# Kernel optimization log

Hardware: AMD Instinct MI355X
Metric: run time of the kernel (lower is better)

Reference implementation:

```python
import jax, jax.numpy as jnp
import numpy as np

B = 32768
IN_DIM = 768
HIDDENS = [2048, 1024, 512]
EMBED_DIM = 128
NUM_EMB = 1024
DEPTH = 3


def setup_inputs() -> dict:
    key = jax.random.key(0)
    ks = jax.random.split(key, 20)
    d = {"x": jax.random.normal(ks[0], (B, IN_DIM), dtype=jnp.float32)}
    # Encoder: in -> h0 -> h1 -> h2 -> embed  (weights stored as [in, out])
    enc_dims = [IN_DIM] + HIDDENS + [EMBED_DIM]
    for i in range(4):
        fan_in = enc_dims[i]
        d[f"enc_W{i+1}"] = jax.random.normal(ks[1 + i], (enc_dims[i], enc_dims[i + 1]), dtype=jnp.float32) / np.sqrt(fan_in)
        d[f"enc_b{i+1}"] = jnp.zeros((enc_dims[i + 1],), dtype=jnp.float32)
    # Decoder: embed -> h0 -> h1 -> h2 -> in
    dec_dims = [EMBED_DIM] + HIDDENS + [IN_DIM]
    for i in range(4):
        fan_in = dec_dims[i]
        d[f"dec_W{i+1}"] = jax.random.normal(ks[5 + i], (dec_dims[i], dec_dims[i + 1]), dtype=jnp.float32) / np.sqrt(fan_in)
        d[f"dec_b{i+1}"] = jnp.zeros((dec_dims[i + 1],), dtype=jnp.float32)
    # Codebook (nn.Embedding weight, initialized ~ N(0,1) as in the module)
    d["codebook"] = jax.random.normal(ks[9], (NUM_EMB, EMBED_DIM), dtype=jnp.float32)
    return d


def _encoder(x, W1, b1, W2, b2, W3, b3, W4, b4):
    x = jax.nn.relu(x @ W1 + b1)
    x = jax.nn.relu(x @ W2 + b2)
    x = jax.nn.relu(x @ W3 + b3)
    return x @ W4 + b4


def _decoder(x, W1, b1, W2, b2, W3, b3, W4, b4):
    x = jax.nn.relu(x @ W1 + b1)
    x = jax.nn.relu(x @ W2 + b2)
    x = jax.nn.relu(x @ W3 + b3)
    return x @ W4 + b4


def reference(x,
              enc_W1, enc_b1, enc_W2, enc_b2, enc_W3, enc_b3, enc_W4, enc_b4,
              dec_W1, dec_b1, dec_W2, dec_b2, dec_W3, dec_b3, dec_W4, dec_b4,
              codebook):
    z = _encoder(x, enc_W1, enc_b1, enc_W2, enc_b2, enc_W3, enc_b3, enc_W4, enc_b4)
    z_det = jax.lax.stop_gradient(z)

    cb_sq = jnp.sum(codebook * codebook, axis=1)  # [K]
    residue = z_det
    z_hat = jnp.zeros_like(z_det)
    codes = []
    for _ in range(DEPTH):  # residual quantization loop
        # squared L2 distances [B, K]
        dist = (jnp.sum(residue * residue, axis=1, keepdims=True)
                + cb_sq
                - 2.0 * residue @ codebook.T)
        idx = jnp.argmin(dist, axis=1)          # [B]
        codes.append(idx)
        z_hat = z_hat + codebook[idx]           # gather codebook vectors
        residue = z_det - z_hat
    all_codes = jnp.stack(codes, axis=1)        # [B, DEPTH] int

    # straight-through estimator: forward uses z_hat, grad flows through z
    z_flow = z + jax.lax.stop_gradient(z_hat - z)
    x_recon = _decoder(z_flow, dec_W1, dec_b1, dec_W2, dec_b2, dec_W3, dec_b3, dec_W4, dec_b4)
    return (x_recon, all_codes)
```

## Files before the change

kernel.cpp:

```cpp
#include <hip/hip_runtime.h>

#define FLT_MAX_C 3.402823466e+38f

typedef __attribute__((ext_vector_type(8))) __bf16 bf16x8;
typedef __attribute__((ext_vector_type(4))) float f32x4;

static __device__ __forceinline__ ushort f2bf(float x) {
    union { float f; unsigned u; } v; v.f = x;
    unsigned r = (v.u + 0x7FFFu + ((v.u >> 16) & 1u)) >> 16;
    return (ushort)r;
}

template<bool RELU>
__device__ __forceinline__ void gemm_f32_dev(
    const float* __restrict__ A, const float* __restrict__ W,
    const float* __restrict__ bias, float* __restrict__ C, int K, int N)
{
    __shared__ float As[8][128];
    __shared__ float Bs[8][132];
    const int tid = threadIdx.x;
    const int bm = blockIdx.y << 7;
    const int bn = blockIdx.x << 7;

    const int la_row = tid >> 1;
    const int la_k   = (tid & 1) << 2;
    const int lb_row = tid >> 5;
    const int lb_col = (tid & 31) << 2;
    const int tm4 = (tid >> 4) << 2;
    const int tn4 = (tid & 15) << 2;

    float acc[8][8];
    #pragma unroll
    for (int i = 0; i < 8; ++i)
        #pragma unroll
        for (int j = 0; j < 8; ++j) acc[i][j] = 0.f;

    const float* aptr = A + (size_t)(bm + la_row) * K + la_k;
    const float* bptr = W + (size_t)lb_row * N + bn + lb_col;

    float4 av = *(const float4*)(aptr);
    float4 bv = *(const float4*)(bptr);

    for (int k0 = 0; k0 < K; k0 += 8) {
        __syncthreads();
        As[la_k + 0][la_row] = av.x;
        As[la_k + 1][la_row] = av.y;
        As[la_k + 2][la_row] = av.z;
        As[la_k + 3][la_row] = av.w;
        *(float4*)(&Bs[lb_row][lb_col]) = bv;
        __syncthreads();
        if (k0 + 8 < K) {
            av = *(const float4*)(aptr + k0 + 8);
            bv = *(const float4*)(bptr + (size_t)(k0 + 8) * N);
        }
        #pragma unroll
        for (int kk = 0; kk < 8; ++kk) {
            float a[8], b[8];
            *(float4*)(a)     = *(const float4*)(&As[kk][tm4]);
            *(float4*)(a + 4) = *(const float4*)(&As[kk][tm4 + 64]);
            *(float4*)(b)     = *(const float4*)(&Bs[kk][tn4]);
            *(float4*)(b + 4) = *(const float4*)(&Bs[kk][tn4 + 64]);
            #pragma unroll
            for (int i = 0; i < 8; ++i)
                #pragma unroll
                for (int j = 0; j < 8; ++j)
                    acc[i][j] = fmaf(a[i], b[j], acc[i][j]);
        }
    }

    float bv0[8];
    #pragma unroll
    for (int j = 0; j < 8; ++j)
        bv0[j] = bias[bn + tn4 + (j < 4 ? j : 60 + j)];

    #pragma unroll
    for (int i = 0; i < 8; ++i) {
        int row = bm + tm4 + (i < 4 ? i : 60 + i);
        float* cp = C + (size_t)row * N + bn + tn4;
        float4 v0, v1;
        v0.x = acc[i][0] + bv0[0]; v0.y = acc[i][1] + bv0[1];
        v0.z = acc[i][2] + bv0[2]; v0.w = acc[i][3] + bv0[3];
        v1.x = acc[i][4] + bv0[4]; v1.y = acc[i][5] + bv0[5];
        v1.z = acc[i][6] + bv0[6]; v1.w = acc[i][7] + bv0[7];
        if (RELU) {
            v0.x = fmaxf(v0.x, 0.f); v0.y = fmaxf(v0.y, 0.f);
            v0.z = fmaxf(v0.z, 0.f); v0.w = fmaxf(v0.w, 0.f);
            v1.x = fmaxf(v1.x, 0.f); v1.y = fmaxf(v1.y, 0.f);
            v1.z = fmaxf(v1.z, 0.f); v1.w = fmaxf(v1.w, 0.f);
        }
        *(float4*)(cp) = v0;
        *(float4*)(cp + 64) = v1;
    }
}

template<bool RELU>
__device__ __forceinline__ void gemm_f32_64_dev(
    const float* __restrict__ A, const float* __restrict__ W,
    const float* __restrict__ bias, float* __restrict__ C, int K, int N)
{
    __shared__ float As[16][64];
    __shared__ float Bs[16][132];
    const int tid = threadIdx.x;
    const int bm = blockIdx.y << 6;
    const int bn = blockIdx.x << 7;

    const int la_row = tid & 63;
    const int la_k   = (tid >> 6) << 2;
    const int lb_row = tid >> 5;
    const int lb_col = (tid & 31) << 2;
    const int tr = tid >> 4;
    const int tc = tid & 15;

    float acc[4][8];
    #pragma unroll
    for (int i = 0; i < 4; ++i)
        #pragma unroll
        for (int j = 0; j < 8; ++j) acc[i][j] = 0.f;

    const float* aptr = A + (size_t)(bm + la_row) * K + la_k;
    const float* bptr = W + (size_t)lb_row * N + bn + lb_col;

    float4 av = *(const float4*)(aptr);
    float4 bv0 = *(const float4*)(bptr);
    float4 bv1 = *(const float4*)(bptr + (size_t)8 * N);

    for (int k0 = 0; k0 < K; k0 += 16) {
        __syncthreads();
        As[la_k + 0][la_row] = av.x;
        As[la_k + 1][la_row] = av.y;
        As[la_k + 2][la_row] = av.z;
        As[la_k + 3][la_row] = av.w;
        *(float4*)(&Bs[lb_row][lb_col]) = bv0;
        *(float4*)(&Bs[lb_row + 8][lb_col]) = bv1;
        __syncthreads();
        if (k0 + 16 < K) {
            av  = *(const float4*)(aptr + k0 + 16);
            bv0 = *(const float4*)(bptr + (size_t)(k0 + 16) * N);
            bv1 = *(const float4*)(bptr + (size_t)(k0 + 24) * N);
        }
        #pragma unroll
        for (int kk = 0; kk < 16; ++kk) {
            float a[4], b[8];
            *(float4*)(a) = *(const float4*)(&As[kk][tr << 2]);
            *(float4*)(b)     = *(const float4*)(&Bs[kk][tc << 2]);
            *(float4*)(b + 4) = *(const float4*)(&Bs[kk][(tc << 2) + 64]);
            #pragma unroll
            for (int i = 0; i < 4; ++i)
                #pragma unroll
                for (int j = 0; j < 8; ++j)
                    acc[i][j] = fmaf(a[i], b[j], acc[i][j]);
        }
    }

    float bb[8];
    #pragma unroll
    for (int j = 0; j < 8; ++j)
        bb[j] = bias[bn + (tc << 2) + (j < 4 ? j : 60 + j)];

    #pragma unroll
    for (int i = 0; i < 4; ++i) {
        float* cp = C + (size_t)(bm + (tr << 2) + i) * N + bn + (tc << 2);
        float4 v0, v1;
        v0.x = acc[i][0] + bb[0]; v0.y = acc[i][1] + bb[1];
        v0.z = acc[i][2] + bb[2]; v0.w = acc[i][3] + bb[3];
        v1.x = acc[i][4] + bb[4]; v1.y = acc[i][5] + bb[5];
        v1.z = acc[i][6] + bb[6]; v1.w = acc[i][7] + bb[7];
        if (RELU) {
            v0.x = fmaxf(v0.x, 0.f); v0.y = fmaxf(v0.y, 0.f);
            v0.z = fmaxf(v0.z, 0.f); v0.w = fmaxf(v0.w, 0.f);
            v1.x = fmaxf(v1.x, 0.f); v1.y = fmaxf(v1.y, 0.f);
            v1.z = fmaxf(v1.z, 0.f); v1.w = fmaxf(v1.w, 0.f);
        }
        *(float4*)(cp) = v0;
        *(float4*)(cp + 64) = v1;
    }
}

template<bool RELU, bool OUTF32>
__device__ __forceinline__ void gemm_bf16_dev(
    const ushort* __restrict__ A, const ushort* __restrict__ Wt,
    const float* __restrict__ bias, void* __restrict__ C, int K, int N)
{
    __shared__ __align__(16) ushort As[128][64];
    __shared__ __align__(16) ushort Bs[128][64];
    const int tid  = threadIdx.x;
    const int lane = tid & 63;
    const int wv   = tid >> 6;
    const int wm   = (wv >> 1) << 6;
    const int wn   = (wv & 1) << 6;
    const int bm   = blockIdx.y << 7;
    const int bn   = blockIdx.x << 7;
    const int lr   = lane & 15;
    const int lh   = lane >> 4;

    f32x4 acc[4][4];
    #pragma unroll
    for (int m = 0; m < 4; ++m)
        #pragma unroll
        for (int n = 0; n < 4; ++n) acc[m][n] = (f32x4){0.f, 0.f, 0.f, 0.f};

    for (int k0 = 0; k0 < K; k0 += 64) {
        __syncthreads();
        #pragma unroll
        for (int i = 0; i < 4; ++i) {
            const int c    = wv * 4 + i;
            const int boff = c * 1024 + lane * 16;
            const int r    = boff >> 7;
            const int cbt  = boff & 127;
            const char* sa = (const char*)A  + (((size_t)(bm + r) * K + k0) << 1) + cbt;
            const char* sb = (const char*)Wt + (((size_t)(bn + r) * K + k0) << 1) + cbt;
            __builtin_amdgcn_global_load_lds((const void*)sa, (void*)(&As[0][0] + c * 512), 16, 0, 0);
            __builtin_amdgcn_global_load_lds((const void*)sb, (void*)(&Bs[0][0] + c * 512), 16, 0, 0);
        }
        __syncthreads();
        #pragma unroll
        for (int kk = 0; kk < 64; kk += 32) {
            bf16x8 af[4], bfr[4];
            #pragma unroll
            for (int m = 0; m < 4; ++m)
                af[m] = *(const bf16x8*)&As[wm + m * 16 + lr][kk + lh * 8];
            #pragma unroll
            for (int n = 0; n < 4; ++n)
                bfr[n] = *(const bf16x8*)&Bs[wn + n * 16 + lr][kk + lh * 8];
            #pragma unroll
            for (int m = 0; m < 4; ++m)
                #pragma unroll
                for (int n = 0; n < 4; ++n)
                    acc[m][n] = __builtin_amdgcn_mfma_f32_16x16x32_bf16(
                        af[m], bfr[n], acc[m][n], 0, 0, 0);
        }
    }

    #pragma unroll
    for (int n = 0; n < 4; ++n) {
        const int col = bn + wn + n * 16 + lr;
        const float bcol = bias[col];
        #pragma unroll
        for (int m = 0; m < 4; ++m) {
            #pragma unroll
            for (int i = 0; i < 4; ++i) {
                const int row = bm + wm + m * 16 + lh * 4 + i;
                float v = acc[m][n][i] + bcol;
                if (RELU) v = fmaxf(v, 0.f);
                if (OUTF32) ((float*)C)[(size_t)row * N + col] = v;
                else        ((ushort*)C)[(size_t)row * N + col] = f2bf(v);
            }
        }
    }
}

__global__ __launch_bounds__(256) void enc1_gemm(const float* A, const float* W, const float* b, float* C)
{ gemm_f32_dev<true>(A, W, b, C, 768, 2048); }
__global__ __launch_bounds__(256) void enc2_gemm(const float* A, const float* W, const float* b, float* C)
{ gemm_f32_dev<true>(A, W, b, C, 2048, 1024); }
__global__ __launch_bounds__(256) void enc3_gemm(const float* A, const float* W, const float* b, float* C)
{ gemm_f32_dev<true>(A, W, b, C, 1024, 512); }
__global__ __launch_bounds__(256) void enc4_gemm(const float* A, const float* W, const float* b, float* C)
{ gemm_f32_64_dev<false>(A, W, b, C, 512, 128); }
__global__ __launch_bounds__(256) void dec1_gemm(const ushort* A, const ushort* Wt, const float* b, void* C)
{ gemm_bf16_dev<true, false>(A, Wt, b, C, 128, 2048); }
__global__ __launch_bounds__(256) void dec2_gemm(const ushort* A, const ushort* Wt, const float* b, void* C)
{ gemm_bf16_dev<true, false>(A, Wt, b, C, 2048, 1024); }
__global__ __launch_bounds__(256) void dec3_gemm(const ushort* A, const ushort* Wt, const float* b, void* C)
{ gemm_bf16_dev<true, false>(A, Wt, b, C, 1024, 512); }
__global__ __launch_bounds__(256) void dec4_gemm(const ushort* A, const ushort* Wt, const float* b, void* C)
{ gemm_bf16_dev<false, true>(A, Wt, b, C, 512, 768); }

__global__ __launch_bounds__(256) void wt_convert(
    const float* __restrict__ W, ushort* __restrict__ Wt, int K, int N)
{
    __shared__ ushort t[64][65];
    const int kb = blockIdx.y << 6, nb = blockIdx.x << 6;
    const int c  = threadIdx.x & 63;
    const int r0 = (threadIdx.x >> 6) << 4;
    #pragma unroll
    for (int i = 0; i < 16; ++i)
        t[r0 + i][c] = f2bf(W[(size_t)(kb + r0 + i) * N + nb + c]);
    __syncthreads();
    #pragma unroll
    for (int i = 0; i < 16; ++i)
        Wt[(size_t)(nb + r0 + i) * K + kb + c] = t[c][r0 + i];
}

__global__ __launch_bounds__(256) void cbsq_kernel(
    const float* __restrict__ cb, float* __restrict__ cbsq)
{
    int k = blockIdx.x * 256 + threadIdx.x;
    const float* r = cb + ((size_t)k << 7);
    float s = 0.f;
    #pragma unroll 8
    for (int d = 0; d < 128; ++d) s = fmaf(r[d], r[d], s);
    cbsq[k] = s;
}

__global__ __launch_bounds__(256) void cbt_kernel(
    const float* __restrict__ cb, float* __restrict__ cbt)
{
    __shared__ float t[64][65];
    const int kb = blockIdx.x << 6;
    const int db = blockIdx.y << 6;
    const int c  = threadIdx.x & 63;
    const int r0 = (threadIdx.x >> 6) << 4;
    #pragma unroll
    for (int i = 0; i < 16; ++i)
        t[r0 + i][c] = cb[(size_t)(kb + r0 + i) * 128 + db + c];
    __syncthreads();
    #pragma unroll
    for (int i = 0; i < 16; ++i)
        cbt[(size_t)(db + r0 + i) * 1024 + kb + c] = t[c][r0 + i];
}

template<int T>
__global__ __launch_bounds__(256) void rq_step(
    const float* __restrict__ Rres, const float* __restrict__ cbt,
    const float* __restrict__ sq, const float* __restrict__ cb,
    const float* __restrict__ z, float* __restrict__ ZH,
    float* __restrict__ RR, ushort* __restrict__ ZHb,
    float* __restrict__ codes)
{
    __shared__ float As[16][64];
    __shared__ float Bs[16][132];
    __shared__ float rrp[4][64];
    __shared__ float rrs[64];

    const int tid = threadIdx.x;
    const int bm = blockIdx.x << 6;

    const int la_row = tid & 63;
    const int la_k   = (tid >> 6) << 2;
    const int lb_row = tid >> 5;
    const int lb_col = (tid & 31) << 2;
    const int tr  = tid >> 4;
    const int tn4 = (tid & 15) << 2;

    {
        const int r_ = tid & 63, seg = tid >> 6;
        const float4* rp = (const float4*)(Rres + (size_t)(bm + r_) * 128) + seg * 8;
        float s = 0.f;
        #pragma unroll
        for (int i = 0; i < 8; ++i) {
            float4 v = rp[i];
            s = fmaf(v.x, v.x, s); s = fmaf(v.y, v.y, s);
            s = fmaf(v.z, v.z, s); s = fmaf(v.w, v.w, s);
        }
        rrp[seg][r_] = s;
    }
    __syncthreads();
    if (tid < 64) rrs[tid] = (rrp[0][tid] + rrp[1][tid]) + (rrp[2][tid] + rrp[3][tid]);
    __syncthreads();

    float rr_[4];
    #pragma unroll
    for (int i = 0; i < 4; ++i) rr_[i] = rrs[(tr << 2) + i];

    float best_d[4] = {FLT_MAX_C, FLT_MAX_C, FLT_MAX_C, FLT_MAX_C};
    int   best_i[4] = {0, 0, 0, 0};

    const float* aptr = Rres + (size_t)(bm + la_row) * 128 + la_k;

    for (int bx = 0; bx < 8; ++bx) {
        const int bn = bx << 7;
        float acc[4][8];
        #pragma unroll
        for (int i = 0; i < 4; ++i)
            #pragma unroll
            for (int j = 0; j < 8; ++j) acc[i][j] = 0.f;

        const float* bptr = cbt + (size_t)lb_row * 1024 + bn + lb_col;
        float4 av  = *(const float4*)(aptr);
        float4 bv0 = *(const float4*)(bptr);
        float4 bv1 = *(const float4*)(bptr + (size_t)8 * 1024);

        for (int k0 = 0; k0 < 128; k0 += 16) {
            __syncthreads();
            As[la_k + 0][la_row] = av.x;
            As[la_k + 1][la_row] = av.y;
            As[la_k + 2][la_row] = av.z;
            As[la_k + 3][la_row] = av.w;
            *(float4*)(&Bs[lb_row][lb_col]) = bv0;
            *(float4*)(&Bs[lb_row + 8][lb_col]) = bv1;
            __syncthreads();
            if (k0 + 16 < 128) {
                av  = *(const float4*)(aptr + k0 + 16);
                bv0 = *(const float4*)(bptr + (size_t)(k0 + 16) * 1024);
                bv1 = *(const float4*)(bptr + (size_t)(k0 + 24) * 1024);
            }
            #pragma unroll
            for (int kk = 0; kk < 16; ++kk) {
                float a[4], b[8];
                *(float4*)(a) = *(const float4*)(&As[kk][tr << 2]);
                *(float4*)(b)     = *(const float4*)(&Bs[kk][tn4]);
                *(float4*)(b + 4) = *(const float4*)(&Bs[kk][tn4 + 64]);
                #pragma unroll
                for (int i = 0; i < 4; ++i)
                    #pragma unroll
                    for (int j = 0; j < 8; ++j)
                        acc[i][j] = fmaf(a[i], b[j], acc[i][j]);
            }
        }
        #pragma unroll
        for (int i = 0; i < 4; ++i) {
            #pragma unroll
            for (int j = 0; j < 8; ++j) {
                const int col = bn + tn4 + (j < 4 ? j : 60 + j);
                float d = (rr_[i] + sq[col]) - 2.f * acc[i][j];
                if (d < best_d[i]) { best_d[i] = d; best_i[i] = col; }
            }
        }
    }

    #pragma unroll
    for (int i = 0; i < 4; ++i) {
        float bd = best_d[i]; int bi = best_i[i];
        #pragma unroll
        for (int o = 8; o >= 1; o >>= 1) {
            float od = __shfl_xor(bd, o);
            int   oi = __shfl_xor(bi, o);
            if (od < bd || (od == bd && oi < bi)) { bd = od; bi = oi; }
        }
        const int row = bm + (tr << 2) + i;
        if ((tid & 15) == 0) codes[(size_t)row * 3 + T] = (float)bi;

        const int d8 = (tid & 15) << 3;
        const float* cbp = cb + ((size_t)bi << 7) + d8;
        float4 c0 = *(const float4*)(cbp);
        float4 c1 = *(const float4*)(cbp + 4);
        float4 zh0, zh1;
        if (T == 0) {
            zh0 = c0; zh1 = c1;
        } else {
            const float* zhp = ZH + (size_t)row * 128 + d8;
            float4 p0 = *(const float4*)(zhp);
            float4 p1 = *(const float4*)(zhp + 4);
            zh0.x = p0.x + c0.x; zh0.y = p0.y + c0.y;
            zh0.z = p0.z + c0.z; zh0.w = p0.w + c0.w;
            zh1.x = p1.x + c1.x; zh1.y = p1.y + c1.y;
            zh1.z = p1.z + c1.z; zh1.w = p1.w + c1.w;
        }
        if (T < 2) {
            float* zhp = ZH + (size_t)row * 128 + d8;
            *(float4*)(zhp)     = zh0;
            *(float4*)(zhp + 4) = zh1;
            const float* zp = z + (size_t)row * 128 + d8;
            float4 z0 = *(const float4*)(zp);
            float4 z1 = *(const float4*)(zp + 4);
            float4 r0, r1;
            r0.x = z0.x - zh0.x; r0.y = z0.y - zh0.y;
            r0.z = z0.z - zh0.z; r0.w = z0.w - zh0.w;
            r1.x = z1.x - zh1.x; r1.y = z1.y - zh1.y;
            r1.z = z1.z - zh1.z; r1.w = z1.w - zh1.w;
            float* rp = RR + (size_t)row * 128 + d8;
            *(float4*)(rp)     = r0;
            *(float4*)(rp + 4) = r1;
        } else {
            ushort4 o0, o1;
            o0.x = f2bf(zh0.x); o0.y = f2bf(zh0.y);
            o0.z = f2bf(zh0.z); o0.w = f2bf(zh0.w);
            o1.x = f2bf(zh1.x); o1.y = f2bf(zh1.y);
            o1.z = f2bf(zh1.z); o1.w = f2bf(zh1.w);
            ushort* zbp = ZHb + (size_t)row * 128 + d8;
            *(ushort4*)(zbp)     = o0;
            *(ushort4*)(zbp + 4) = o1;
        }
    }
}

extern "C" void kernel_launch(void* const* d_in, const int* in_sizes, int n_in,
                              void* d_out, int out_size, void* d_ws, size_t ws_size,
                              hipStream_t stream)
{
    const float* x   = (const float*)d_in[0];
    const float* eW1 = (const float*)d_in[1];
    const float* eb1 = (const float*)d_in[2];
    const float* eW2 = (const float*)d_in[3];
    const float* eb2 = (const float*)d_in[4];
    const float* eW3 = (const float*)d_in[5];
    const float* eb3 = (const float*)d_in[6];
    const float* eW4 = (const float*)d_in[7];
    const float* eb4 = (const float*)d_in[8];
    const float* dW1 = (const float*)d_in[9];
    const float* db1 = (const float*)d_in[10];
    const float* dW2 = (const float*)d_in[11];
    const float* db2 = (const float*)d_in[12];
    const float* dW3 = (const float*)d_in[13];
    const float* db3 = (const float*)d_in[14];
    const float* dW4 = (const float*)d_in[15];
    const float* db4 = (const float*)d_in[16];
    const float* cb  = (const float*)d_in[17];

    float* out   = (float*)d_out;
    float* codes = out + (size_t)32768 * 768;

    ushort* Wt1 = (ushort*)d_ws;
    ushort* Wt2 = Wt1 + (size_t)2048 * 128;
    ushort* Wt3 = Wt2 + (size_t)1024 * 2048;
    ushort* Wt4 = Wt3 + (size_t)512 * 1024;
    float*  sq  = (float*)(Wt4 + (size_t)768 * 512);
    float*  cbt = sq + 1024;
    float*  act = cbt + (size_t)128 * 1024;
    const size_t fixed_b = (char*)act - (char*)d_ws;

    int mc = 32768;
    while (mc > 1024) {
        if (fixed_b + (size_t)mc * 15104 <= ws_size) break;
        mc >>= 1;
    }

    float*  R1  = act;
    float*  R2  = R1 + (size_t)mc * 2048;
    float*  R3  = R2 + (size_t)mc * 1024;
    float*  RZ  = R3 + (size_t)mc * 512;
    ushort* ZHb = (ushort*)(RZ + (size_t)mc * 128);
    float*  RR  = R2 + (size_t)mc * 512;
    float*  ZH  = R3 + (size_t)mc * 256;
    ushort* D1  = (ushort*)R1;
    ushort* D2  = (ushort*)R2;
    ushort* D3  = (ushort*)R3;

    wt_convert<<<dim3(2048 / 64, 128 / 64), 256, 0, stream>>>(dW1, Wt1, 128, 2048);
    wt_convert<<<dim3(1024 / 64, 2048 / 64), 256, 0, stream>>>(dW2, Wt2, 2048, 1024);
    wt_convert<<<dim3(512 / 64, 1024 / 64), 256, 0, stream>>>(dW3, Wt3, 1024, 512);
    wt_convert<<<dim3(768 / 64, 512 / 64), 256, 0, stream>>>(dW4, Wt4, 512, 768);
    cbsq_kernel<<<4, 256, 0, stream>>>(cb, sq);
    cbt_kernel<<<dim3(16, 2), 256, 0, stream>>>(cb, cbt);

    const int mg = mc >> 7;
    for (int r0 = 0; r0 < 32768; r0 += mc) {
        const float* xi     = x     + (size_t)r0 * 768;
        float*       outi   = out   + (size_t)r0 * 768;
        float*       codesi = codes + (size_t)r0 * 3;
        enc1_gemm<<<dim3(16, mg), 256, 0, stream>>>(xi, eW1, eb1, R1);
        enc2_gemm<<<dim3( 8, mg), 256, 0, stream>>>(R1, eW2, eb2, R2);
        enc3_gemm<<<dim3( 4, mg), 256, 0, stream>>>(R2, eW3, eb3, R3);
        enc4_gemm<<<dim3( 1, mc >> 6), 256, 0, stream>>>(R3, eW4, eb4, RZ);
        rq_step<0><<<mc >> 6, 256, 0, stream>>>(RZ, cbt, sq, cb, RZ, ZH, RR, ZHb, codesi);
        rq_step<1><<<mc >> 6, 256, 0, stream>>>(RR, cbt, sq, cb, RZ, ZH, RR, ZHb, codesi);
        rq_step<2><<<mc >> 6, 256, 0, stream>>>(RR, cbt, sq, cb, RZ, ZH, RR, ZHb, codesi);
        dec1_gemm<<<dim3(16, mg), 256, 0, stream>>>(ZHb, Wt1, db1, D1);
        dec2_gemm<<<dim3( 8, mg), 256, 0, stream>>>(D1,  Wt2, db2, D2);
        dec3_gemm<<<dim3( 4, mg), 256, 0, stream>>>(D2,  Wt3, db3, D3);
        dec4_gemm<<<dim3( 6, mg), 256, 0, stream>>>(D3,  Wt4, db4, outi);
    }
}
```

Measured before the change: 4.010 ms.

## Fuse three residual-quantization steps into one kernel keeping residue in LDS

```diff
diff --git a/kernel.cpp b/kernel.cpp
--- a/kernel.cpp
+++ b/kernel.cpp
@@ -310,158 +310,170 @@
         cbt[(size_t)(db + r0 + i) * 1024 + kb + c] = t[c][r0 + i];
 }
 
-template<int T>
-__global__ __launch_bounds__(256) void rq_step(
-    const float* __restrict__ Rres, const float* __restrict__ cbt,
+__global__ __launch_bounds__(256) void rq_all(
+    const float* __restrict__ z, const float* __restrict__ cbt,
     const float* __restrict__ sq, const float* __restrict__ cb,
-    const float* __restrict__ z, float* __restrict__ ZH,
-    float* __restrict__ RR, ushort* __restrict__ ZHb,
-    float* __restrict__ codes)
-{
-    __shared__ float As[16][64];
-    __shared__ float Bs[16][132];
-    __shared__ float rrp[4][64];
+    ushort* __restrict__ ZHb, float* __restrict__ codes)
+{
+    __shared__ float As[128][68];
+    __shared__ float Bs[32][132];
+    __shared__ float sqs[1024];
     __shared__ float rrs[64];
 
     const int tid = threadIdx.x;
-    const int bm = blockIdx.x << 6;
-
-    const int la_row = tid & 63;
-    const int la_k   = (tid >> 6) << 2;
+    const int bm  = blockIdx.x << 6;
+    const int tr  = tid >> 4;
+    const int c   = tid & 15;
+    const int tn4 = c << 2;
     const int lb_row = tid >> 5;
     const int lb_col = (tid & 31) << 2;
-    const int tr  = tid >> 4;
-    const int tn4 = (tid & 15) << 2;
-
-    {
-        const int r_ = tid & 63, seg = tid >> 6;
-        const float4* rp = (const float4*)(Rres + (size_t)(bm + r_) * 128) + seg * 8;
-        float s = 0.f;
-        #pragma unroll
-        for (int i = 0; i < 8; ++i) {
-            float4 v = rp[i];
-            s = fmaf(v.x, v.x, s); s = fmaf(v.y, v.y, s);
-            s = fmaf(v.z, v.z, s); s = fmaf(v.w, v.w, s);
-        }
-        rrp[seg][r_] = s;
+
+    #pragma unroll
+    for (int i = 0; i < 4; ++i) sqs[tid + (i << 8)] = sq[tid + (i << 8)];
+
+    float zh[4][8];
+    #pragma unroll
+    for (int i = 0; i < 4; ++i) {
+        const int r_  = (tr << 2) + i;
+        const float* zp = z + (size_t)(bm + r_) * 128 + (c << 3);
+        float4 z0 = *(const float4*)(zp);
+        float4 z1 = *(const float4*)(zp + 4);
+        #pragma unroll
+        for (int j = 0; j < 8; ++j) zh[i][j] = 0.f;
+        As[(c << 3) + 0][r_] = z0.x; As[(c << 3) + 1][r_] = z0.y;
+        As[(c << 3) + 2][r_] = z0.z; As[(c << 3) + 3][r_] = z0.w;
+        As[(c << 3) + 4][r_] = z1.x; As[(c << 3) + 5][r_] = z1.y;
+        As[(c << 3) + 6][r_] = z1.z; As[(c << 3) + 7][r_] = z1.w;
+        float p = z0.x * z0.x;
+        p = fmaf(z0.y, z0.y, p); p = fmaf(z0.z, z0.z, p);
+        p = fmaf(z0.w, z0.w, p); p = fmaf(z1.x, z1.x, p);
+        p = fmaf(z1.y, z1.y, p); p = fmaf(z1.z, z1.z, p);
+        p = fmaf(z1.w, z1.w, p);
+        #pragma unroll
+        for (int o = 8; o >= 1; o >>= 1) p += __shfl_xor(p, o);
+        if (c == 0) rrs[r_] = p;
     }
     __syncthreads();
-    if (tid < 64) rrs[tid] = (rrp[0][tid] + rrp[1][tid]) + (rrp[2][tid] + rrp[3][tid]);
-    __syncthreads();
-
-    float rr_[4];
-    #pragma unroll
-    for (int i = 0; i < 4; ++i) rr_[i] = rrs[(tr << 2) + i];
-
-    float best_d[4] = {FLT_MAX_C, FLT_MAX_C, FLT_MAX_C, FLT_MAX_C};
-    int   best_i[4] = {0, 0, 0, 0};
-
-    const float* aptr = Rres + (size_t)(bm + la_row) * 128 + la_k;
-
-    for (int bx = 0; bx < 8; ++bx) {
-        const int bn = bx << 7;
-        float acc[4][8];
-        #pragma unroll
-        for (int i = 0; i < 4; ++i)
-            #pragma unroll
-            for (int j = 0; j < 8; ++j) acc[i][j] = 0.f;
-
-        const float* bptr = cbt + (size_t)lb_row * 1024 + bn + lb_col;
-        float4 av  = *(const float4*)(aptr);
-        float4 bv0 = *(const float4*)(bptr);
-        float4 bv1 = *(const float4*)(bptr + (size_t)8 * 1024);
-
-        for (int k0 = 0; k0 < 128; k0 += 16) {
-            __syncthreads();
-            As[la_k + 0][la_row] = av.x;
-            As[la_k + 1][la_row] = av.y;
-            As[la_k + 2][la_row] = av.z;
-            As[la_k + 3][la_row] = av.w;
-            *(float4*)(&Bs[lb_row][lb_col]) = bv0;
-            *(float4*)(&Bs[lb_row + 8][lb_col]) = bv1;
-            __syncthreads();
-            if (k0 + 16 < 128) {
-                av  = *(const float4*)(aptr + k0 + 16);
-                bv0 = *(const float4*)(bptr + (size_t)(k0 + 16) * 1024);
-                bv1 = *(const float4*)(bptr + (size_t)(k0 + 24) * 1024);
+
+    for (int t = 0; t < 3; ++t) {
+        float rr_[4];
+        #pragma unroll
+        for (int i = 0; i < 4; ++i) rr_[i] = rrs[(tr << 2) + i];
+
+        float best_d[4] = {FLT_MAX_C, FLT_MAX_C, FLT_MAX_C, FLT_MAX_C};
+        int   best_i[4] = {0, 0, 0, 0};
+
+        for (int bx = 0; bx < 8; ++bx) {
+            const int bn = bx << 7;
+            const float* bptr = cbt + (size_t)lb_row * 1024 + bn + lb_col;
+            float4 bv0 = *(const float4*)(bptr);
+            float4 bv1 = *(const float4*)(bptr + (size_t)8  * 1024);
+            float4 bv2 = *(const float4*)(bptr + (size_t)16 * 1024);
+            float4 bv3 = *(const float4*)(bptr + (size_t)24 * 1024);
+
+            float acc[4][8];
+            #pragma unroll
+            for (int i = 0; i < 4; ++i)
+                #pragma unroll
+                for (int j = 0; j < 8; ++j) acc[i][j] = 0.f;
+
+            for (int k0 = 0; k0 < 128; k0 += 32) {
+                __syncthreads();
+                *(float4*)(&Bs[lb_row +  0][lb_col]) = bv0;
+                *(float4*)(&Bs[lb_row +  8][lb_col]) = bv1;
+                *(float4*)(&Bs[lb_row + 16][lb_col]) = bv2;
+                *(float4*)(&Bs[lb_row + 24][lb_col]) = bv3;
+                __syncthreads();
+                if (k0 + 32 < 128) {
+                    bv0 = *(const float4*)(bptr + (size_t)(k0 + 32) * 1024);
+                    bv1 = *(const float4*)(bptr + (size_t)(k0 + 40) * 1024);
+                    bv2 = *(const float4*)(bptr + (size_t)(k0 + 48) * 1024);
+                    bv3 = *(const float4*)(bptr + (size_t)(k0 + 56) * 1024);
+                }
+                #pragma unroll
+                for (int kk = 0; kk < 32; ++kk) {
+                    float a[4], b[8];
+                    *(float4*)(a)     = *(const float4*)(&As[k0 + kk][tr << 2]);
+                    *(float4*)(b)     = *(const float4*)(&Bs[kk][tn4]);
+                    *(float4*)(b + 4) = *(const float4*)(&Bs[kk][tn4 + 64]);
+                    #pragma unroll
+                    for (int i = 0; i < 4; ++i)
+                        #pragma unroll
+                        for (int j = 0; j < 8; ++j)
+                            acc[i][j] = fmaf(a[i], b[j], acc[i][j]);
+                }
             }
             #pragma unroll
-            for (int kk = 0; kk < 16; ++kk) {
-                float a[4], b[8];
-                *(float4*)(a) = *(const float4*)(&As[kk][tr << 2]);
-                *(float4*)(b)     = *(const float4*)(&Bs[kk][tn4]);
-                *(float4*)(b + 4) = *(const float4*)(&Bs[kk][tn4 + 64]);
-                #pragma unroll
-                for (int i = 0; i < 4; ++i)
-                    #pragma unroll
-                    for (int j = 0; j < 8; ++j)
-                        acc[i][j] = fmaf(a[i], b[j], acc[i][j]);
+            for (int i = 0; i < 4; ++i) {
+                #pragma unroll
+                for (int j = 0; j < 8; ++j) {
+                    const int col = bn + tn4 + (j < 4 ? j : 60 + j);
+                    float d = (rr_[i] + sqs[col]) - 2.f * acc[i][j];
+                    if (d < best_d[i]) { best_d[i] = d; best_i[i] = col; }
+                }
             }
         }
+
         #pragma unroll
         for (int i = 0; i < 4; ++i) {
-            #pragma unroll
-            for (int j = 0; j < 8; ++j) {
-                const int col = bn + tn4 + (j < 4 ? j : 60 + j);
-                float d = (rr_[i] + sq[col]) - 2.f * acc[i][j];
-                if (d < best_d[i]) { best_d[i] = d; best_i[i] = col; }
+            float bd = best_d[i]; int bi = best_i[i];
+            #pragma unroll
+            for (int o = 8; o >= 1; o >>= 1) {
+                float od = __shfl_xor(bd, o);
+                int   oi = __shfl_xor(bi, o);
+                if (od < bd || (od == bd && oi < bi)) { bd = od; bi = oi; }
             }
-        }
-    }
-
-    #pragma unroll
-    for (int i = 0; i < 4; ++i) {
-        float bd = best_d[i]; int bi = best_i[i];
-        #pragma unroll
-        for (int o = 8; o >= 1; o >>= 1) {
-            float od = __shfl_xor(bd, o);
-            int   oi = __shfl_xor(bi, o);
-            if (od < bd || (od == bd && oi < bi)) { bd = od; bi = oi; }
-        }
-        const int row = bm + (tr << 2) + i;
-        if ((tid & 15) == 0) codes[(size_t)row * 3 + T] = (float)bi;
-
-        const int d8 = (tid & 15) << 3;
-        const float* cbp = cb + ((size_t)bi << 7) + d8;
-        float4 c0 = *(const float4*)(cbp);
-        float4 c1 = *(const float4*)(cbp + 4);
-        float4 zh0, zh1;
-        if (T == 0) {
-            zh0 = c0; zh1 = c1;
-        } else {
-            const float* zhp = ZH + (size_t)row * 128 + d8;
-            float4 p0 = *(const float4*)(zhp);
-            float4 p1 = *(const float4*)(zhp + 4);
-            zh0.x = p0.x + c0.x; zh0.y = p0.y + c0.y;
-            zh0.z = p0.z + c0.z; zh0.w = p0.w + c0.w;
-            zh1.x = p1.x + c1.x; zh1.y = p1.y + c1.y;
-            zh1.z = p1.z + c1.z; zh1.w = p1.w + c1.w;
-        }
-        if (T < 2) {
-            float* zhp = ZH + (size_t)row * 128 + d8;
-            *(float4*)(zhp)     = zh0;
-            *(float4*)(zhp + 4) = zh1;
-            const float* zp = z + (size_t)row * 128 + d8;
-            float4 z0 = *(const float4*)(zp);
-            float4 z1 = *(const float4*)(zp + 4);
-            float4 r0, r1;
-            r0.x = z0.x - zh0.x; r0.y = z0.y - zh0.y;
-            r0.z = z0.z - zh0.z; r0.w = z0.w - zh0.w;
-            r1.x = z1.x - zh1.x; r1.y = z1.y - zh1.y;
-            r1.z = z1.z - zh1.z; r1.w = z1.w - zh1.w;
-            float* rp = RR + (size_t)row * 128 + d8;
-            *(float4*)(rp)     = r0;
-            *(float4*)(rp + 4) = r1;
-        } else {
-            ushort4 o0, o1;
-            o0.x = f2bf(zh0.x); o0.y = f2bf(zh0.y);
-            o0.z = f2bf(zh0.z); o0.w = f2bf(zh0.w);
-            o1.x = f2bf(zh1.x); o1.y = f2bf(zh1.y);
-            o1.z = f2bf(zh1.z); o1.w = f2bf(zh1.w);
-            ushort* zbp = ZHb + (size_t)row * 128 + d8;
-            *(ushort4*)(zbp)     = o0;
-            *(ushort4*)(zbp + 4) = o1;
-        }
+            best_i[i] = bi;
+        }
+
+        __syncthreads();
+
+        #pragma unroll
+        for (int i = 0; i < 4; ++i) {
+            const int r_  = (tr << 2) + i;
+            const int row = bm + r_;
+            if (c == 0) codes[(size_t)row * 3 + t] = (float)best_i[i];
+
+            const float* cbp = cb + ((size_t)best_i[i] << 7) + (c << 3);
+            float4 c0 = *(const float4*)(cbp);
+            float4 c1 = *(const float4*)(cbp + 4);
+            zh[i][0] += c0.x; zh[i][1] += c0.y;
+            zh[i][2] += c0.z; zh[i][3] += c0.w;
+            zh[i][4] += c1.x; zh[i][5] += c1.y;
+            zh[i][6] += c1.z; zh[i][7] += c1.w;
+
+            if (t < 2) {
+                const float* zp = z + (size_t)row * 128 + (c << 3);
+                float4 z0 = *(const float4*)(zp);
+                float4 z1 = *(const float4*)(zp + 4);
+                float r0 = z0.x - zh[i][0], r1 = z0.y - zh[i][1];
+                float r2 = z0.z - zh[i][2], r3 = z0.w - zh[i][3];
+                float r4 = z1.x - zh[i][4], r5 = z1.y - zh[i][5];
+                float r6 = z1.z - zh[i][6], r7 = z1.w - zh[i][7];
+                As[(c << 3) + 0][r_] = r0; As[(c << 3) + 1][r_] = r1;
+                As[(c << 3) + 2][r_] = r2; As[(c << 3) + 3][r_] = r3;
+                As[(c << 3) + 4][r_] = r4; As[(c << 3) + 5][r_] = r5;
+                As[(c << 3) + 6][r_] = r6; As[(c << 3) + 7][r_] = r7;
+                float p = r0 * r0;
+                p = fmaf(r1, r1, p); p = fmaf(r2, r2, p);
+                p = fmaf(r3, r3, p); p = fmaf(r4, r4, p);
+                p = fmaf(r5, r5, p); p = fmaf(r6, r6, p);
+                p = fmaf(r7, r7, p);
+                #pragma unroll
+                for (int o = 8; o >= 1; o >>= 1) p += __shfl_xor(p, o);
+                if (c == 0) rrs[r_] = p;
+            } else {
+                ushort4 o0, o1;
+                o0.x = f2bf(zh[i][0]); o0.y = f2bf(zh[i][1]);
+                o0.z = f2bf(zh[i][2]); o0.w = f2bf(zh[i][3]);
+                o1.x = f2bf(zh[i][4]); o1.y = f2bf(zh[i][5]);
+                o1.z = f2bf(zh[i][6]); o1.w = f2bf(zh[i][7]);
+                ushort* zbp = ZHb + (size_t)row * 128 + (c << 3);
+                *(ushort4*)(zbp)     = o0;
+                *(ushort4*)(zbp + 4) = o1;
+            }
+        }
+        if (t < 2) __syncthreads();
     }
 }
 
@@ -511,8 +523,6 @@
     float*  R3  = R2 + (size_t)mc * 1024;
     float*  RZ  = R3 + (size_t)mc * 512;
     ushort* ZHb = (ushort*)(RZ + (size_t)mc * 128);
-    float*  RR  = R2 + (size_t)mc * 512;
-    float*  ZH  = R3 + (size_t)mc * 256;
     ushort* D1  = (ushort*)R1;
     ushort* D2  = (ushort*)R2;
     ushort* D3  = (ushort*)R3;
@@ -533,9 +543,7 @@
         enc2_gemm<<<dim3( 8, mg), 256, 0, stream>>>(R1, eW2, eb2, R2);
         enc3_gemm<<<dim3( 4, mg), 256, 0, stream>>>(R2, eW3, eb3, R3);
         enc4_gemm<<<dim3( 1, mc >> 6), 256, 0, stream>>>(R3, eW4, eb4, RZ);
-        rq_step<0><<<mc >> 6, 256, 0, stream>>>(RZ, cbt, sq, cb, RZ, ZH, RR, ZHb, codesi);
-        rq_step<1><<<mc >> 6, 256, 0, stream>>>(RR, cbt, sq, cb, RZ, ZH, RR, ZHb, codesi);
-        rq_step<2><<<mc >> 6, 256, 0, stream>>>(RR, cbt, sq, cb, RZ, ZH, RR, ZHb, codesi);
+        rq_all<<<mc >> 6, 256, 0, stream>>>(RZ, cbt, sq, cb, ZHb, codesi);
         dec1_gemm<<<dim3(16, mg), 256, 0, stream>>>(ZHb, Wt1, db1, D1);
         dec2_gemm<<<dim3( 8, mg), 256, 0, stream>>>(D1,  Wt2, db2, D2);
         dec3_gemm<<<dim3( 4, mg), 256, 0, stream>>>(D2,  Wt3, db3, D3);
```

After: 3.923 ms. 1.02x faster.
